# Performance work log

Measured on AMD Instinct MI355X. Metric: run time of the kernel, lower is better.

Reference implementation:

```python
import jax, jax.numpy as jnp
import numpy as np
from jax import lax

N = 2048          # batch_size*2 (two views)
DIM_IN = 1024     # stub encoder input width
DIM_FEAT = 2048
DIM = 128
C = 1000          # num_classes
Q = 8             # queue_size_per_cls
K_POS = 4         # select_num_pos
K_NEG = 1024      # select_num_neg
EPS = 1e-5


def setup_inputs() -> dict:
    key = jax.random.key(0)
    ks = jax.random.split(key, 12)
    img = jax.random.normal(ks[0], (N, DIM_IN), dtype=jnp.float32)
    labels = jax.random.randint(ks[1], (N,), 0, C)
    # buffers
    ql = jax.random.normal(ks[2], (DIM, Q * C), dtype=jnp.float32)
    queue_list = ql / jnp.linalg.norm(ql, axis=0, keepdims=True)
    queue_ptr = jnp.zeros((C,), dtype=jnp.int32)
    pos_index = jnp.asarray(np.arange(Q * C).reshape(C, Q))
    cols = np.arange(Q * (C - 1))
    # skip class-i block: indices >= Q*i shift up by Q
    neg_index = jnp.asarray(cols[None, :] + Q * ((cols[None, :] // Q) >= np.arange(C)[:, None]))
    # params (stub encoder + mlp head + classifier)
    s = 0.02
    enc_W = s * jax.random.normal(ks[3], (DIM_IN, DIM_FEAT), dtype=jnp.float32)
    enc_b = jnp.zeros((DIM_FEAT,), dtype=jnp.float32)
    mlp_W1 = s * jax.random.normal(ks[4], (DIM_FEAT, DIM_FEAT), dtype=jnp.float32)
    mlp_b1 = jnp.zeros((DIM_FEAT,), dtype=jnp.float32)
    bn_gamma = jnp.ones((DIM_FEAT,), dtype=jnp.float32)
    bn_beta = jnp.zeros((DIM_FEAT,), dtype=jnp.float32)
    mlp_W2 = s * jax.random.normal(ks[5], (DIM_FEAT, DIM), dtype=jnp.float32)
    mlp_b2 = jnp.zeros((DIM,), dtype=jnp.float32)
    lin_W = s * jax.random.normal(ks[6], (DIM_FEAT, C), dtype=jnp.float32)
    lin_b = jnp.zeros((C,), dtype=jnp.float32)
    return dict(img=img, labels=labels, queue_list=queue_list, queue_ptr=queue_ptr,
                pos_index=pos_index, neg_index=neg_index,
                enc_W=enc_W, enc_b=enc_b, mlp_W1=mlp_W1, mlp_b1=mlp_b1,
                bn_gamma=bn_gamma, bn_beta=bn_beta, mlp_W2=mlp_W2, mlp_b2=mlp_b2,
                lin_W=lin_W, lin_b=lin_b)


def _offdiag_idx(n):
    # idx[i,j] = j + (j >= i): gather columns of an [n,n] matrix skipping the diagonal
    cols = jnp.arange(n - 1)
    return cols[None, :] + (cols[None, :] >= jnp.arange(n)[:, None]).astype(cols.dtype)


def reference(img, labels, queue_list, queue_ptr, pos_index, neg_index,
              enc_W, enc_b, mlp_W1, mlp_b1, bn_gamma, bn_beta,
              mlp_W2, mlp_b2, lin_W, lin_b):
    # encoder (stub) -> mid_feat
    mid = img @ enc_W + enc_b                                  # [N, DIM_FEAT]
    # mlp: Linear -> BatchNorm1d (training stats) -> ReLU -> Linear
    h = mid @ mlp_W1 + mlp_b1
    mu = jnp.mean(h, axis=0)
    var = jnp.var(h, axis=0)
    h = (h - mu) * lax.rsqrt(var + EPS) * bn_gamma + bn_beta
    h = jax.nn.relu(h)
    feat = h @ mlp_W2 + mlp_b2
    feat = feat / jnp.linalg.norm(feat, axis=1, keepdims=True)  # [N, DIM]
    logit_cls = mid @ lin_W + lin_b                             # [N, C]

    # queue similarities (queue is detached in the original)
    ql = lax.stop_gradient(queue_list)
    sim_q = feat @ ql                                           # [N, Q*C]
    sim_pos = jnp.take_along_axis(sim_q, pos_index[labels], axis=1)   # [N, Q]
    sim_neg = jnp.take_along_axis(sim_q, neg_index[labels], axis=1)   # [N, Q*(C-1)]
    pos_sel = -lax.top_k(-sim_pos, K_POS)[0]     # hardest (smallest) positives
    neg_sel = lax.top_k(sim_neg, K_NEG)[0]       # hardest (largest) negatives

    # in-batch similarities with diagonal removed
    sim_b = feat @ feat.T                                       # [N, N]
    off = _offdiag_idx(sim_b.shape[0])
    sim_b_off = jnp.take_along_axis(sim_b, off, axis=1)         # [N, N-1]
    sim_con = jnp.concatenate([sim_b_off, pos_sel, neg_sel], axis=1)

    lab_b = (labels[:, None] == labels[None, :]).astype(jnp.float32)
    lab_off = jnp.take_along_axis(lab_b, off, axis=1)
    labels_con = jnp.concatenate([lab_off, jnp.ones_like(pos_sel), jnp.zeros_like(neg_sel)], axis=1)

    # dequeue/enqueue: sequential per-sample scatter into per-class circular buffer
    feat_k = lax.stop_gradient(feat[: feat.shape[0] // 2])
    labels_k = labels[: labels.shape[0] // 2]

    def step(carry, x):
        ql_, qp_ = carry
        f, c = x
        ptr = qp_[c]
        real = c * Q + ptr
        ql_ = ql_.at[:, real].set(f)
        qp_ = qp_.at[c].set((ptr + 1) % Q)
        return (ql_, qp_), None

    (queue_list_new, queue_ptr_new), _ = lax.scan(step, (queue_list, queue_ptr), (feat_k, labels_k))
    return sim_con, labels_con, logit_cls, queue_list_new, queue_ptr_new
```

## Files before the change

kernel.cpp:

```cpp
#include <hip/hip_runtime.h>
#include <cstdint>
#include <cstddef>

#define NB      2048
#define DIN     1024
#define DF      2048
#define DM      128
#define NCLS    1000
#define QQ      8
#define QC      8000
#define QCP     8064
#define NLP     1024
#define CONW    3075
#define FSPLIT  8
#define NBUCK   8192

using float4v = __attribute__((ext_vector_type(4))) float;
using bf16x8  = __attribute__((ext_vector_type(8))) __bf16;

#define GLB_AS __attribute__((address_space(1)))
#define LDS_AS __attribute__((address_space(3)))

__device__ __forceinline__ unsigned short f2bf(float f) {
  unsigned int u = __float_as_uint(f);
  u += 0x7fffu + ((u >> 16) & 1u);
  return (unsigned short)(u >> 16);
}
__device__ __forceinline__ float bf2f(unsigned short u) {
  return __uint_as_float(((unsigned int)u) << 16);
}

__device__ __forceinline__ bf16x8 ld_frag8(const unsigned short* p) {
  union { uint4 u; bf16x8 b; } cv;
  cv.u = *(const uint4*)p;
  return cv.b;
}

__device__ __forceinline__ void gload_lds16(const unsigned short* g, unsigned short* l) {
  __builtin_amdgcn_global_load_lds((const GLB_AS unsigned int*)g,
                                   (LDS_AS unsigned int*)l, 16, 0, 0);
}

__global__ void conv_bf16_kernel(const float* __restrict__ in, unsigned short* __restrict__ out, int n) {
  int idx = blockIdx.x * 256 + threadIdx.x;
  if (idx < n) out[idx] = f2bf(in[idx]);
}

struct TDescs {
  const float* src[5];
  unsigned short* dst[5];
  int K[5], N[5], nx[5], ky[5];
};
__global__ void transpose_all_kernel(TDescs d) {
  const int mid = blockIdx.y;
  const int nx = d.nx[mid];
  const int kb32 = blockIdx.x / nx, nb32 = blockIdx.x % nx;
  if (kb32 >= d.ky[mid]) return;
  const float* src = d.src[mid];
  unsigned short* dst = d.dst[mid];
  const int K = d.K[mid], N = d.N[mid];
  const int nb = nb32 * 32, kb = kb32 * 32;
  __shared__ float tile[32][33];
  int tx = threadIdx.x, ty = threadIdx.y;
#pragma unroll
  for (int r = 0; r < 32; r += 8) {
    int k = kb + ty + r, n = nb + tx;
    tile[ty + r][tx] = (n < N) ? src[(size_t)k * N + n] : 0.f;
  }
  __syncthreads();
#pragma unroll
  for (int r = 0; r < 32; r += 8) {
    int n = nb + ty + r, k = kb + tx;
    dst[(size_t)n * K + k] = f2bf(tile[tx][ty + r]);
  }
}

template<int OUT_MODE, bool HAS_BIAS, bool BN_STATS>
__global__ __launch_bounds__(256) void gemm_bt_kernel(
    const unsigned short* __restrict__ A,
    const unsigned short* __restrict__ Bt,
    const float* __restrict__ bias,
    const float* __restrict__ bias2,
    void* __restrict__ Cout,
    void* __restrict__ Cout2,
    int lda, int klen, int ldc, int n_store,
    float* __restrict__ ps, float* __restrict__ ps2)
{
  __shared__ __align__(16) unsigned short As[2][128][32];
  __shared__ __align__(16) unsigned short Bs[2][128][32];
  const int m0 = blockIdx.y * 128, n0 = blockIdx.x * 128;
  const int z  = blockIdx.z;
  const int tid = threadIdx.x;
  const int lane = tid & 63, w = tid >> 6;
  const int wm = (w >> 1) * 64, wn = (w & 1) * 64;
  const int lrow = lane & 15, lq = lane >> 4;

  const unsigned short* Abase = A  + (size_t)m0 * lda + z * klen;
  const unsigned short* Bbase = Bt + (size_t)n0 * lda + z * klen;

  const int c0 = tid, c1 = tid + 256;
  const size_t off0 = (size_t)(c0 >> 2) * lda + (c0 & 3) * 8;
  const size_t off1 = (size_t)(c1 >> 2) * lda + (c1 & 3) * 8;

  float4v acc[4][4];
#pragma unroll
  for (int i = 0; i < 4; ++i)
#pragma unroll
    for (int j = 0; j < 4; ++j)
      acc[i][j] = (float4v){0.f, 0.f, 0.f, 0.f};

  auto stage = [&](int buf, int k0) {
    gload_lds16(Abase + off0 + k0, &As[buf][0][0] + c0 * 8);
    gload_lds16(Abase + off1 + k0, &As[buf][0][0] + c1 * 8);
    gload_lds16(Bbase + off0 + k0, &Bs[buf][0][0] + c0 * 8);
    gload_lds16(Bbase + off1 + k0, &Bs[buf][0][0] + c1 * 8);
  };

  const int NKT = klen / 32;
  stage(0, 0);
  for (int t = 0; t < NKT; ++t) {
    __syncthreads();
    if (t + 1 < NKT) stage((t + 1) & 1, (t + 1) * 32);
    const int b = t & 1;
    bf16x8 af[4], bfr[4];
#pragma unroll
    for (int i = 0; i < 4; ++i) af[i]  = ld_frag8(&As[b][wm + i * 16 + lrow][lq * 8]);
#pragma unroll
    for (int j = 0; j < 4; ++j) bfr[j] = ld_frag8(&Bs[b][wn + j * 16 + lrow][lq * 8]);
#pragma unroll
    for (int i = 0; i < 4; ++i)
#pragma unroll
      for (int j = 0; j < 4; ++j)
        acc[i][j] = __builtin_amdgcn_mfma_f32_16x16x32_bf16(af[i], bfr[j], acc[i][j], 0, 0, 0);
  }

  const bool is2nd = (OUT_MODE == 3 && n0 >= DF) || (OUT_MODE == 4 && n0 >= QCP);
  const bool do_bn = BN_STATS && !is2nd;

  float* cs  = (float*)&As[0][0][0];
  float* cs2 = cs + 128;
  if (do_bn) {
    __syncthreads();
    if (tid < 256) cs[tid] = 0.f;
    __syncthreads();
  }

  float*          outf  = (float*)Cout          + (size_t)z * NB * ldc;
  unsigned short* outh  = (unsigned short*)Cout + (size_t)z * NB * ldc;
  float*          outf2 = (float*)Cout2;

#pragma unroll
  for (int j = 0; j < 4; ++j) {
    int gcol = n0 + wn + j * 16 + lrow;
    float bv = 0.f;
    if (OUT_MODE == 3) {
      if (!is2nd) bv = bias[gcol];
      else if (gcol - DF < NCLS) bv = bias2[gcol - DF];
    } else if (HAS_BIAS && gcol < n_store) bv = bias[gcol];
    float sj = 0.f, s2j = 0.f;
#pragma unroll
    for (int i = 0; i < 4; ++i) {
#pragma unroll
      for (int r = 0; r < 4; ++r) {
        int grow = m0 + wm + i * 16 + lq * 4 + r;
        float val = acc[i][j][r] + bv;
        if (do_bn) { sj += val; s2j += val * val; }
        if (OUT_MODE == 0) {
          if (gcol < n_store) outf[(size_t)grow * ldc + gcol] = val;
        } else if (OUT_MODE == 1) {
          if (gcol < n_store) outh[(size_t)grow * ldc + gcol] = f2bf(val);
        } else if (OUT_MODE == 3) {
          if (!is2nd) outh[(size_t)grow * DF + gcol] = f2bf(val);
          else if (gcol - DF < NCLS) outf2[(size_t)grow * NCLS + (gcol - DF)] = val;
        } else if (OUT_MODE == 4) {
          if (!is2nd) { if (gcol < QC) outh[(size_t)grow * QC + gcol] = f2bf(val); }
          else {
            int gc2 = gcol - QCP;
            if (gc2 != grow) outf2[(size_t)grow * CONW + gc2 - (gc2 > grow)] = val;
          }
        }
      }
    }
    if (do_bn) {
      atomicAdd(&cs [wn + j * 16 + lrow], sj);
      atomicAdd(&cs2[wn + j * 16 + lrow], s2j);
    }
  }
  if (do_bn) {
    __syncthreads();
    if (tid < 128) {
      ps [(size_t)blockIdx.y * DF + n0 + tid] = cs[tid];
      ps2[(size_t)blockIdx.y * DF + n0 + tid] = cs2[tid];
    }
  }
}

__global__ void bn_finish_kernel(const float* __restrict__ ps, const float* __restrict__ ps2,
                                 const float* __restrict__ gamma, const float* __restrict__ beta,
                                 float* __restrict__ scale, float* __restrict__ bias) {
  int j = blockIdx.x * 256 + threadIdx.x;
  float s = 0.f, s2 = 0.f;
  for (int b = 0; b < 16; ++b) { s += ps[b * DF + j]; s2 += ps2[b * DF + j]; }
  float mu  = s  * (1.f / NB);
  float var = s2 * (1.f / NB) - mu * mu;
  float sc = gamma[j] * rsqrtf(var + 1e-5f);
  scale[j] = sc;
  bias[j]  = beta[j] - mu * sc;
}

__global__ void bn_apply_kernel(const unsigned short* __restrict__ h, const float* __restrict__ scale,
                                const float* __restrict__ bias, unsigned short* __restrict__ hb) {
  int base = (blockIdx.x * 256 + threadIdx.x) * 8;
  int j = base & (DF - 1);
  uint4 u = *(const uint4*)(h + base);
  unsigned int uu[4] = {u.x, u.y, u.z, u.w};
  unsigned int rr[4];
#pragma unroll
  for (int e = 0; e < 4; ++e) {
    int col = j + 2 * e;
    float lo = bf2f((unsigned short)(uu[e] & 0xffffu));
    float hi = bf2f((unsigned short)(uu[e] >> 16));
    lo = fmaxf(lo * scale[col] + bias[col], 0.f);
    hi = fmaxf(hi * scale[col + 1] + bias[col + 1], 0.f);
    rr[e] = (unsigned int)f2bf(lo) | ((unsigned int)f2bf(hi) << 16);
  }
  uint4 o; o.x = rr[0]; o.y = rr[1]; o.z = rr[2]; o.w = rr[3];
  *(uint4*)(hb + base) = o;
}

__global__ void feat_reduce_norm_kernel(const float* __restrict__ part, const float* __restrict__ b2,
                                        float* __restrict__ fo, unsigned short* __restrict__ fb) {
  int row = blockIdx.x, t = threadIdx.x;
  float v0 = b2[t], v1 = b2[64 + t];
#pragma unroll
  for (int s = 0; s < FSPLIT; ++s) {
    const float* p = part + (size_t)s * NB * DM + (size_t)row * DM;
    v0 += p[t]; v1 += p[64 + t];
  }
  float ss = v0 * v0 + v1 * v1;
#pragma unroll
  for (int o = 32; o > 0; o >>= 1) ss += __shfl_xor(ss, o);
  float inv = rsqrtf(ss);
  v0 *= inv; v1 *= inv;
  fo[row * DM + t] = v0;       fo[row * DM + 64 + t] = v1;
  fb[row * DM + t] = f2bf(v0); fb[row * DM + 64 + t] = f2bf(v1);
}

__global__ __launch_bounds__(256) void topk_kernel(const unsigned short* __restrict__ sim_qb,
                                                   const int* __restrict__ labels,
                                                   float* __restrict__ out_simcon) {
  __shared__ unsigned int hist[NBUCK];
  __shared__ float sbuf[1024];
  __shared__ unsigned int wtot[4];
  __shared__ int s_tb;

  const int row = blockIdx.x;
  const int c = labels[row];
  const int t = threadIdx.x;
  const int w = t >> 6, lane = t & 63;

  uint4* h4 = (uint4*)hist;
  uint4 z4; z4.x = z4.y = z4.z = z4.w = 0u;
#pragma unroll
  for (int i = 0; i < 8; ++i) h4[t + 256 * i] = z4;

  float vals[32];
  float pvals[QQ];
  const unsigned short* rp = sim_qb + (size_t)row * QC;
#pragma unroll
  for (int j = 0; j < 4; ++j) {
    const int cls = j * 256 + t;
    uint4 u4 = *(const uint4*)(rp + j * 2048 + t * 8);
    const unsigned int uu[4] = {u4.x, u4.y, u4.z, u4.w};
    const bool masked = (cls >= NCLS) || (cls == c);
#pragma unroll
    for (int e = 0; e < 4; ++e) {
      float lo = bf2f((unsigned short)(uu[e] & 0xffffu));
      float hi = bf2f((unsigned short)(uu[e] >> 16));
      if (cls == c) { pvals[2 * e] = lo; pvals[2 * e + 1] = hi; }
      vals[j * 8 + 2 * e]     = masked ? -4.f : lo;
      vals[j * 8 + 2 * e + 1] = masked ? -4.f : hi;
    }
  }
  __syncthreads();

#pragma unroll
  for (int i = 0; i < 32; ++i) {
    float v = vals[i];
    if (v > -3.f) {
      int b = (int)((v + 1.0f) * 4096.0f);
      b = min(max(b, 0), NBUCK - 1);
      atomicAdd(&hist[b], 1u);
    }
  }
  __syncthreads();

  unsigned int cnt[32];
#pragma unroll
  for (int k = 0; k < 8; ++k) {
    uint4 u = h4[t * 8 + k];
    cnt[4 * k] = u.x; cnt[4 * k + 1] = u.y; cnt[4 * k + 2] = u.z; cnt[4 * k + 3] = u.w;
  }
  unsigned int chunktot = 0;
#pragma unroll
  for (int i = 0; i < 32; ++i) chunktot += cnt[i];

  unsigned int s = chunktot;
#pragma unroll
  for (int off = 1; off < 64; off <<= 1) {
    unsigned int v = __shfl_down(s, off);
    if (lane + off < 64) s += v;
  }
  if (lane == 0) wtot[w] = s;
  __syncthreads();
  unsigned int wsfx = 0;
#pragma unroll
  for (int ww = 0; ww < 4; ++ww) if (ww > w) wsfx += wtot[ww];
  unsigned int S = wsfx + s - chunktot;

  unsigned int ofsv[32];
#pragma unroll
  for (int i = 31; i >= 0; --i) {
    unsigned int cb = cnt[i];
    ofsv[i] = S;
    unsigned int Sincl = S + cb;
    if (S < 1024u && Sincl >= 1024u) s_tb = t * 32 + i;
    S = Sincl;
  }
#pragma unroll
  for (int k = 0; k < 8; ++k) {
    uint4 u;
    u.x = ofsv[4 * k]; u.y = ofsv[4 * k + 1]; u.z = ofsv[4 * k + 2]; u.w = ofsv[4 * k + 3];
    h4[t * 8 + k] = u;
  }
  __syncthreads();

  const int tb = s_tb;
#pragma unroll
  for (int i = 0; i < 32; ++i) {
    float v = vals[i];
    if (v > -3.f) {
      int b = (int)((v + 1.0f) * 4096.0f);
      b = min(max(b, 0), NBUCK - 1);
      if (b >= tb) {
        unsigned int p = atomicAdd(&hist[b], 1u);
        if (p < 1024u) sbuf[p] = v;
      }
    }
  }
  __syncthreads();

  float* orow = out_simcon + (size_t)row * CONW;
  for (int idx = t; idx < 1024; idx += 256) orow[2051 + idx] = sbuf[idx];
  if (t == (c & 255) && (c >> 8) < 4 && (c >> 8) * 256 + t == c) {
    for (int a2 = 1; a2 < QQ; ++a2) {
      float key = pvals[a2]; int b2 = a2 - 1;
      while (b2 >= 0 && pvals[b2] > key) { pvals[b2 + 1] = pvals[b2]; --b2; }
      pvals[b2 + 1] = key;
    }
#pragma unroll
    for (int s2 = 0; s2 < 4; ++s2) orow[2047 + s2] = pvals[s2];
  }
}

__global__ void labels_con_kernel(const int* __restrict__ labels, float* __restrict__ out_lab) {
  int i = blockIdx.x;
  int li = labels[i];
  for (int j = threadIdx.x; j < CONW; j += 256) {
    float v;
    if (j < NB - 1)      v = (labels[j + (j >= i)] == li) ? 1.f : 0.f;
    else if (j < NB + 3) v = 1.f;
    else                 v = 0.f;
    out_lab[(size_t)i * CONW + j] = v;
  }
}

__global__ void queue_scan_kernel(const int* __restrict__ labels, const int* __restrict__ qptr_in,
                                  int* __restrict__ writer, float* __restrict__ qptr_out) {
  __shared__ int wloc[QQ];
  const int c = blockIdx.x;
  const int lane = threadIdx.x;
  if (lane < QQ) wloc[lane] = -1;
  __syncthreads();
  const int p0 = qptr_in[c];
  int cnt = 0;
#pragma unroll
  for (int t = 0; t < (NB / 2) / 64; ++t) {
    int i = t * 64 + lane;
    bool pred = (labels[i] == c);
    unsigned long long mask = __ballot(pred);
    if (pred) {
      int rank = __popcll(mask & ((1ull << lane) - 1ull));
      int slot = (p0 + cnt + rank) & (QQ - 1);
      atomicMax(&wloc[slot], i);
    }
    cnt += __popcll(mask);
  }
  __syncthreads();
  if (lane < QQ) writer[c * QQ + lane] = wloc[lane];
  if (lane == 0) qptr_out[c] = (float)((p0 + cnt) & (QQ - 1));
}

__global__ void queue_write_kernel(const int* __restrict__ writer, const float* __restrict__ feat,
                                   const float* __restrict__ qin, float* __restrict__ qout) {
  int idx = blockIdx.x * 256 + threadIdx.x;
  int col = idx % QC;
  int d   = idx / QC;
  int wsrc = writer[col];
  float v = (wsrc >= 0) ? feat[(size_t)wsrc * DM + d] : qin[idx];
  qout[idx] = v;
}

extern "C" void kernel_launch(void* const* d_in, const int* in_sizes, int n_in,
                              void* d_out, int out_size, void* d_ws, size_t ws_size,
                              hipStream_t stream) {
  const float* img     = (const float*)d_in[0];
  const int*   labels  = (const int*)  d_in[1];
  const float* queue_l = (const float*)d_in[2];
  const int*   queue_p = (const int*)  d_in[3];
  const float* enc_W   = (const float*)d_in[6];
  const float* enc_b   = (const float*)d_in[7];
  const float* W1      = (const float*)d_in[8];
  const float* b1      = (const float*)d_in[9];
  const float* gamma   = (const float*)d_in[10];
  const float* beta    = (const float*)d_in[11];
  const float* W2      = (const float*)d_in[12];
  const float* b2      = (const float*)d_in[13];
  const float* linW    = (const float*)d_in[14];
  const float* linb    = (const float*)d_in[15];

  float* out        = (float*)d_out;
  float* out_simcon = out;
  float* out_labcon = out + (size_t)NB * CONW;
  float* out_logit  = out + (size_t)2 * NB * CONW;
  float* out_qlist  = out_logit + (size_t)NB * NCLS;
  float* out_qptr   = out_qlist + (size_t)DM * QC;

  char* wsp = (char*)d_ws;
  size_t off = 0;
  auto alloc = [&](size_t bytes) -> void* {
    void* p = wsp + off;
    off += (bytes + 255) & ~(size_t)255;
    return p;
  };
  unsigned short* img_bf  = (unsigned short*)alloc((size_t)NB * DIN * 2);
  unsigned short* encWt   = (unsigned short*)alloc((size_t)DF * DIN * 2);
  unsigned short* W1t     = (unsigned short*)alloc((size_t)DF * DF * 2);
  unsigned short* linWt   = (unsigned short*)alloc((size_t)NLP * DF * 2);
  unsigned short* W2t     = (unsigned short*)alloc((size_t)DM * DF * 2);
  unsigned short* qlt     = (unsigned short*)alloc((size_t)QCP * DM * 2);
  unsigned short* feat_bf = (unsigned short*)alloc((size_t)NB * DM * 2);
  unsigned short* mid_bf  = (unsigned short*)alloc((size_t)NB * DF * 2);
  unsigned short* h_pbf   = (unsigned short*)alloc((size_t)NB * DF * 2);
  unsigned short* h_bf    = (unsigned short*)alloc((size_t)NB * DF * 2);
  float*          part_s  = (float*)alloc((size_t)16 * DF * 4);
  float*          part_s2 = (float*)alloc((size_t)16 * DF * 4);
  float*          bn_sc   = (float*)alloc((size_t)DF * 4);
  float*          bn_bi   = (float*)alloc((size_t)DF * 4);
  float*          feat_part=(float*)alloc((size_t)FSPLIT * NB * DM * 4);
  float*          feat_f  = (float*)alloc((size_t)NB * DM * 4);
  unsigned short* sim_qb  = (unsigned short*)alloc((size_t)NB * QC * 2 + 512);
  int*            writer  = (int*)alloc((size_t)QC * 4);

  dim3 blk256(256);
  dim3 tblk(32, 8);

  conv_bf16_kernel<<<dim3((NB * DIN) / 256), blk256, 0, stream>>>(img, img_bf, NB * DIN);
  TDescs td;
  td.src[0] = enc_W;  td.dst[0] = encWt; td.K[0] = DIN; td.N[0] = DF;   td.nx[0] = DF / 32;   td.ky[0] = DIN / 32;
  td.src[1] = W1;     td.dst[1] = W1t;   td.K[1] = DF;  td.N[1] = DF;   td.nx[1] = DF / 32;   td.ky[1] = DF / 32;
  td.src[2] = W2;     td.dst[2] = W2t;   td.K[2] = DF;  td.N[2] = DM;   td.nx[2] = DM / 32;   td.ky[2] = DF / 32;
  td.src[3] = linW;   td.dst[3] = linWt; td.K[3] = DF;  td.N[3] = NCLS; td.nx[3] = NLP / 32;  td.ky[3] = DF / 32;
  td.src[4] = queue_l;td.dst[4] = qlt;   td.K[4] = DM;  td.N[4] = QC;   td.nx[4] = QCP / 32;  td.ky[4] = DM / 32;
  transpose_all_kernel<<<dim3(4096, 5), tblk, 0, stream>>>(td);

  gemm_bt_kernel<1, true, false><<<dim3(DF / 128, NB / 128), blk256, 0, stream>>>(
      img_bf, encWt, enc_b, nullptr, mid_bf, nullptr, DIN, DIN, DF, DF, nullptr, nullptr);

  gemm_bt_kernel<3, true, true><<<dim3((DF + NLP) / 128, NB / 128), blk256, 0, stream>>>(
      mid_bf, W1t, b1, linb, h_pbf, out_logit, DF, DF, DF, DF, part_s, part_s2);

  bn_finish_kernel<<<dim3(DF / 256), blk256, 0, stream>>>(part_s, part_s2, gamma, beta, bn_sc, bn_bi);
  bn_apply_kernel<<<dim3((NB * DF) / 2048), blk256, 0, stream>>>(h_pbf, bn_sc, bn_bi, h_bf);

  gemm_bt_kernel<0, false, false><<<dim3(DM / 128, NB / 128, FSPLIT), blk256, 0, stream>>>(
      h_bf, W2t, nullptr, nullptr, feat_part, nullptr, DF, DF / FSPLIT, DM, DM, nullptr, nullptr);

  feat_reduce_norm_kernel<<<dim3(NB), dim3(64), 0, stream>>>(feat_part, b2, feat_f, feat_bf);

  gemm_bt_kernel<4, false, false><<<dim3((QCP + NB) / 128, NB / 128), blk256, 0, stream>>>(
      feat_bf, qlt, nullptr, nullptr, sim_qb, out_simcon, DM, DM, QC, QC, nullptr, nullptr);

  topk_kernel<<<dim3(NB), blk256, 0, stream>>>(sim_qb, labels, out_simcon);

  labels_con_kernel<<<dim3(NB), blk256, 0, stream>>>(labels, out_labcon);

  queue_scan_kernel<<<dim3(NCLS), dim3(64), 0, stream>>>(labels, queue_p, writer, out_qptr);
  queue_write_kernel<<<dim3((DM * QC) / 256), blk256, 0, stream>>>(writer, feat_f, queue_l, out_qlist);
}
```

Before: 326.7 us.

## Deepen GEMM LDS pipeline to four stages with explicit vmcnt waits

Templates the bf16 GEMM on pipeline depth and uses a 4-buffer LDS ring for the encoder, MLP and feat GEMMs. Each stage is gated by explicit s_waitcnt vmcnt counts and a raw s_barrier instead of __syncthreads, so more global-to-LDS loads stay in flight. It also doubles the split-K factor for the feat GEMM. This costs twice the LDS per block, which can lower occupancy, and the hand-tuned vmcnt values are fragile.

Result: no change. 332.6 us (+1.8%).

```diff
diff --git a/kernel.cpp b/kernel.cpp
--- a/kernel.cpp
+++ b/kernel.cpp
@@ -12,7 +12,7 @@
 #define QCP     8064
 #define NLP     1024
 #define CONW    3075
-#define FSPLIT  8
+#define FSPLIT  16
 #define NBUCK   8192
 
 using float4v = __attribute__((ext_vector_type(4))) float;
@@ -75,7 +75,7 @@
   }
 }
 
-template<int OUT_MODE, bool HAS_BIAS, bool BN_STATS>
+template<int OUT_MODE, bool HAS_BIAS, bool BN_STATS, int PIPE>
 __global__ __launch_bounds__(256) void gemm_bt_kernel(
     const unsigned short* __restrict__ A,
     const unsigned short* __restrict__ Bt,
@@ -86,8 +86,8 @@
     int lda, int klen, int ldc, int n_store,
     float* __restrict__ ps, float* __restrict__ ps2)
 {
-  __shared__ __align__(16) unsigned short As[2][128][32];
-  __shared__ __align__(16) unsigned short Bs[2][128][32];
+  __shared__ __align__(16) unsigned short As[PIPE][128][32];
+  __shared__ __align__(16) unsigned short Bs[PIPE][128][32];
   const int m0 = blockIdx.y * 128, n0 = blockIdx.x * 128;
   const int z  = blockIdx.z;
   const int tid = threadIdx.x;
@@ -117,11 +117,22 @@
   };
 
   const int NKT = klen / 32;
-  stage(0, 0);
+#pragma unroll
+  for (int p = 0; p < PIPE - 1; ++p)
+    if (p < NKT) stage(p & (PIPE - 1), p * 32);
+
   for (int t = 0; t < NKT; ++t) {
-    __syncthreads();
-    if (t + 1 < NKT) stage((t + 1) & 1, (t + 1) * 32);
-    const int b = t & 1;
+    __builtin_amdgcn_sched_barrier(0);
+    if constexpr (PIPE == 2) {
+      asm volatile("s_waitcnt vmcnt(0)" ::: "memory");
+    } else {
+      if (t + 3 <= NKT)      asm volatile("s_waitcnt vmcnt(8)" ::: "memory");
+      else if (t == NKT - 2) asm volatile("s_waitcnt vmcnt(4)" ::: "memory");
+      else                   asm volatile("s_waitcnt vmcnt(0)" ::: "memory");
+    }
+    __builtin_amdgcn_s_barrier();
+    if (t + PIPE - 1 < NKT) stage((t + PIPE - 1) & (PIPE - 1), (t + PIPE - 1) * 32);
+    const int b = t & (PIPE - 1);
     bf16x8 af[4], bfr[4];
 #pragma unroll
     for (int i = 0; i < 4; ++i) af[i]  = ld_frag8(&As[b][wm + i * 16 + lrow][lq * 8]);
@@ -474,21 +485,21 @@
   td.src[4] = queue_l;td.dst[4] = qlt;   td.K[4] = DM;  td.N[4] = QC;   td.nx[4] = QCP / 32;  td.ky[4] = DM / 32;
   transpose_all_kernel<<<dim3(4096, 5), tblk, 0, stream>>>(td);
 
-  gemm_bt_kernel<1, true, false><<<dim3(DF / 128, NB / 128), blk256, 0, stream>>>(
+  gemm_bt_kernel<1, true, false, 4><<<dim3(DF / 128, NB / 128), blk256, 0, stream>>>(
       img_bf, encWt, enc_b, nullptr, mid_bf, nullptr, DIN, DIN, DF, DF, nullptr, nullptr);
 
-  gemm_bt_kernel<3, true, true><<<dim3((DF + NLP) / 128, NB / 128), blk256, 0, stream>>>(
+  gemm_bt_kernel<3, true, true, 4><<<dim3((DF + NLP) / 128, NB / 128), blk256, 0, stream>>>(
       mid_bf, W1t, b1, linb, h_pbf, out_logit, DF, DF, DF, DF, part_s, part_s2);
 
   bn_finish_kernel<<<dim3(DF / 256), blk256, 0, stream>>>(part_s, part_s2, gamma, beta, bn_sc, bn_bi);
   bn_apply_kernel<<<dim3((NB * DF) / 2048), blk256, 0, stream>>>(h_pbf, bn_sc, bn_bi, h_bf);
 
-  gemm_bt_kernel<0, false, false><<<dim3(DM / 128, NB / 128, FSPLIT), blk256, 0, stream>>>(
+  gemm_bt_kernel<0, false, false, 4><<<dim3(DM / 128, NB / 128, FSPLIT), blk256, 0, stream>>>(
       h_bf, W2t, nullptr, nullptr, feat_part, nullptr, DF, DF / FSPLIT, DM, DM, nullptr, nullptr);
 
   feat_reduce_norm_kernel<<<dim3(NB), dim3(64), 0, stream>>>(feat_part, b2, feat_f, feat_bf);
 
-  gemm_bt_kernel<4, false, false><<<dim3((QCP + NB) / 128, NB / 128), blk256, 0, stream>>>(
+  gemm_bt_kernel<4, false, false, 2><<<dim3((QCP + NB) / 128, NB / 128), blk256, 0, stream>>>(
       feat_bf, qlt, nullptr, nullptr, sim_qb, out_simcon, DM, DM, QC, QC, nullptr, nullptr);
 
   topk_kernel<<<dim3(NB), blk256, 0, stream>>>(sim_qb, labels, out_simcon);
```

## Double GEMM K-tile to 64 with XOR-swizzled LDS layout

Applied to the files above, without the earlier changes.

The bf16 GEMM now stages a K-tile of 64 instead of 32 per pipeline step, which halves the number of barriers and loop iterations and issues two MFMA sub-steps per tile. The LDS tile columns are XOR-swizzled by row so fragment reads spread across banks instead of colliding. This doubles LDS use per block (64 KB for the two buffers), which can lower occupancy. It also requires every klen to be a multiple of 64, and the epilogue reuse of As as scratch has to stay within the new size.

New measurement: 311.0 us. 1.05x faster.

```diff
diff --git a/kernel.cpp b/kernel.cpp
--- a/kernel.cpp
+++ b/kernel.cpp
@@ -86,21 +86,28 @@
     int lda, int klen, int ldc, int n_store,
     float* __restrict__ ps, float* __restrict__ ps2)
 {
-  __shared__ __align__(16) unsigned short As[2][128][32];
-  __shared__ __align__(16) unsigned short Bs[2][128][32];
+  __shared__ __align__(16) unsigned short As[2][128][64];
+  __shared__ __align__(16) unsigned short Bs[2][128][64];
   const int m0 = blockIdx.y * 128, n0 = blockIdx.x * 128;
   const int z  = blockIdx.z;
   const int tid = threadIdx.x;
   const int lane = tid & 63, w = tid >> 6;
   const int wm = (w >> 1) * 64, wn = (w & 1) * 64;
   const int lrow = lane & 15, lq = lane >> 4;
+  const int r7 = lrow & 7;
 
   const unsigned short* Abase = A  + (size_t)m0 * lda + z * klen;
   const unsigned short* Bbase = Bt + (size_t)n0 * lda + z * klen;
 
-  const int c0 = tid, c1 = tid + 256;
-  const size_t off0 = (size_t)(c0 >> 2) * lda + (c0 & 3) * 8;
-  const size_t off1 = (size_t)(c1 >> 2) * lda + (c1 & 3) * 8;
+  int cc[4]; size_t goff[4];
+#pragma unroll
+  for (int q = 0; q < 4; ++q) {
+    int c = tid + 256 * q;
+    int row = c >> 3;
+    int ucol = (c & 7) ^ (row & 7);
+    cc[q] = c;
+    goff[q] = (size_t)row * lda + ucol * 8;
+  }
 
   float4v acc[4][4];
 #pragma unroll
@@ -110,28 +117,35 @@
       acc[i][j] = (float4v){0.f, 0.f, 0.f, 0.f};
 
   auto stage = [&](int buf, int k0) {
-    gload_lds16(Abase + off0 + k0, &As[buf][0][0] + c0 * 8);
-    gload_lds16(Abase + off1 + k0, &As[buf][0][0] + c1 * 8);
-    gload_lds16(Bbase + off0 + k0, &Bs[buf][0][0] + c0 * 8);
-    gload_lds16(Bbase + off1 + k0, &Bs[buf][0][0] + c1 * 8);
+#pragma unroll
+    for (int q = 0; q < 4; ++q)
+      gload_lds16(Abase + goff[q] + k0, &As[buf][0][0] + cc[q] * 8);
+#pragma unroll
+    for (int q = 0; q < 4; ++q)
+      gload_lds16(Bbase + goff[q] + k0, &Bs[buf][0][0] + cc[q] * 8);
   };
 
-  const int NKT = klen / 32;
+  const int NKT = klen / 64;
   stage(0, 0);
   for (int t = 0; t < NKT; ++t) {
     __syncthreads();
-    if (t + 1 < NKT) stage((t + 1) & 1, (t + 1) * 32);
+    if (t + 1 < NKT) stage((t + 1) & 1, (t + 1) * 64);
     const int b = t & 1;
-    bf16x8 af[4], bfr[4];
-#pragma unroll
-    for (int i = 0; i < 4; ++i) af[i]  = ld_frag8(&As[b][wm + i * 16 + lrow][lq * 8]);
-#pragma unroll
-    for (int j = 0; j < 4; ++j) bfr[j] = ld_frag8(&Bs[b][wn + j * 16 + lrow][lq * 8]);
-#pragma unroll
-    for (int i = 0; i < 4; ++i)
+#pragma unroll
+    for (int kk = 0; kk < 2; ++kk) {
+      bf16x8 af[4], bfr[4];
+#pragma unroll
+      for (int i = 0; i < 4; ++i)
+        af[i]  = ld_frag8(&As[b][wm + i * 16 + lrow][(((kk << 2) + lq) ^ r7) << 3]);
 #pragma unroll
       for (int j = 0; j < 4; ++j)
-        acc[i][j] = __builtin_amdgcn_mfma_f32_16x16x32_bf16(af[i], bfr[j], acc[i][j], 0, 0, 0);
+        bfr[j] = ld_frag8(&Bs[b][wn + j * 16 + lrow][(((kk << 2) + lq) ^ r7) << 3]);
+#pragma unroll
+      for (int i = 0; i < 4; ++i)
+#pragma unroll
+        for (int j = 0; j < 4; ++j)
+          acc[i][j] = __builtin_amdgcn_mfma_f32_16x16x32_bf16(af[i], bfr[j], acc[i][j], 0, 0, 0);
+    }
   }
 
   const bool is2nd = (OUT_MODE == 3 && n0 >= DF) || (OUT_MODE == 4 && n0 >= QCP);
```
